# Kernel tuning notes

Measured on AMD Instinct MI355X. Metric: run time of the kernel, lower is better.

Reference implementation:

```python
import jax, jax.numpy as jnp
import numpy as np

B, S, T = 32, 512, 32
EMB, HID = 256, 512
VOCAB, OOV = 50000, 100


def setup_inputs() -> dict:
    key = jax.random.key(0)
    ks = jax.random.split(key, 20)
    g = lambda k, shape: (0.02 * jax.random.normal(k, shape)).astype(jnp.float32)
    return {
        "dec_input_ids": jax.random.randint(ks[0], (B, T), 0, VOCAB),
        "enc_ids_ext": jax.random.randint(ks[1], (B, S), 0, VOCAB + OOV),
        "encoder_states": jax.random.normal(ks[2], (B, S, HID), jnp.float32),
        "enc_padding_mask": jnp.ones((B, S), jnp.float32),
        "init_h": jax.random.normal(ks[3], (B, HID), jnp.float32),
        "init_c": jax.random.normal(ks[4], (B, HID), jnp.float32),
        "embeddings": g(ks[5], (VOCAB, EMB)),
        "W_enc": g(ks[6], (HID, HID)),
        "b_enc": jnp.zeros((HID,), jnp.float32),
        "W_attn": g(ks[7], (2 * HID, HID)),
        "v": g(ks[8], (HID,)),
        "w_cov": g(ks[9], (HID,)),
        "b_cov": jnp.zeros((HID,), jnp.float32),
        "W_x": g(ks[10], (EMB + HID, HID)),
        "W_out": g(ks[11], (2 * HID, HID)),
        "Wk": g(ks[12], (HID, 4 * HID)),
        "Wr": g(ks[13], (HID, 4 * HID)),
        "b_lstm": jnp.zeros((4 * HID,), jnp.float32),
        "W_pgen": g(ks[14], (4 * HID, 1)),
        "W_proj": g(ks[15], (HID, VOCAB)),
        "b_proj": jnp.zeros((VOCAB,), jnp.float32),
    }


def reference(dec_input_ids, enc_ids_ext, encoder_states, enc_padding_mask,
              init_h, init_c, embeddings, W_enc, b_enc, W_attn, v, w_cov,
              b_cov, W_x, W_out, Wk, Wr, b_lstm, W_pgen, W_proj, b_proj):
    Bq = encoder_states.shape[0]
    # 1x1 conv over [B,S,1,H] == pointwise linear
    enc_feat = jnp.einsum('bsh,hv->bsv', encoder_states, W_enc) + b_enc  # [B,S,V]
    emb = jnp.swapaxes(embeddings[dec_input_ids], 0, 1)  # [T,B,E]
    rows = jnp.arange(Bq)[:, None]

    def lstm(x, h, c):
        z = x @ Wk + h @ Wr + b_lstm
        i, f, g_, o = jnp.split(z, 4, axis=-1)
        c2 = jax.nn.sigmoid(f) * c + jax.nn.sigmoid(i) * jnp.tanh(g_)
        h2 = jax.nn.sigmoid(o) * jnp.tanh(c2)
        return h2, c2

    def attend(h, c, cov):
        dec_feat = jnp.concatenate([h, c], -1) @ W_attn  # [B,V]
        feats = enc_feat + dec_feat[:, None, :]
        if cov is not None:  # 1x1 conv on coverage [B,S,1,1] -> [B,S,V]
            feats = feats + cov[..., None] * w_cov + b_cov
        e = jnp.sum(v * jnp.tanh(feats), -1)  # [B,S]
        attn = jax.nn.softmax(e, axis=-1) * enc_padding_mask
        attn = attn / jnp.sum(attn, -1, keepdims=True)
        ctx = jnp.einsum('bs,bsv->bv', attn, enc_feat)
        return ctx, attn

    def decode(inp, h, c, ctx, cov):
        x = jnp.concatenate([inp, ctx], -1) @ W_x
        h, c = lstm(x, h, c)
        ctx, attn = attend(h, c, cov)
        p_gen = jax.nn.sigmoid(jnp.concatenate([ctx, h, c, x], -1) @ W_pgen)  # [B,1]
        out = jnp.concatenate([h, ctx], -1) @ W_out
        vocab_dist = jax.nn.softmax(out @ W_proj + b_proj, axis=-1)
        ext = jnp.concatenate([p_gen * vocab_dist,
                               jnp.zeros((Bq, OOV), vocab_dist.dtype)], -1)
        final = ext.at[rows, enc_ids_ext].add((1.0 - p_gen) * attn)
        return h, c, ctx, attn, p_gen, final

    # step 0: coverage starts as None, initialized from first attn dist
    ctx0 = jnp.zeros((Bq, HID), encoder_states.dtype)
    h, c, ctx, attn0, pg0, final0 = decode(emb[0], init_h, init_c, ctx0, None)
    cov = attn0

    def scan_step(carry, inp):
        h, c, ctx, cov = carry
        h, c, ctx, attn, pg, final = decode(inp, h, c, ctx, cov)
        return (h, c, ctx, cov + attn), final

    (_, _, _, cov), finals = jax.lax.scan(scan_step, (h, c, ctx, cov), emb[1:])
    final_dists = jnp.concatenate([final0[None], finals], axis=0)  # [T,B,VOCAB+OOV]
    return final_dists
```

## Files before the change

kernel.cpp:

```cpp
#include <hip/hip_runtime.h>
#include <math.h>

#define Bq 32
#define Sq 512
#define Tq 32
#define EMBq 256
#define HIDq 512
#define VOCABq 50000
#define OOVq 100
#define VEXTq (VOCABq + OOVq)
#define HALF_N 25088

typedef unsigned short u16;
typedef unsigned long long u64;
typedef __attribute__((ext_vector_type(8))) short bf16x8;
typedef __attribute__((ext_vector_type(4))) float f32x4;

__device__ __forceinline__ float sigmoidf_(float x){ return 1.0f/(1.0f+__expf(-x)); }
__device__ __forceinline__ float tanhf_(float x){ return 1.0f - 2.0f/(__expf(2.0f*x)+1.0f); }

__device__ __forceinline__ u16 f2bf(float x){
  union{float f; unsigned u;} v; v.f=x;
  unsigned r = v.u + 0x7FFFu + ((v.u>>16)&1u);
  return (u16)(r>>16);
}
__device__ __forceinline__ float bf2f(u16 h){
  union{unsigned u; float f;} v; v.u = ((unsigned)h)<<16; return v.f;
}

__device__ __forceinline__ float ld1(const float* p){
  return __hip_atomic_load((float*)p, __ATOMIC_RELAXED, __HIP_MEMORY_SCOPE_AGENT);
}
__device__ __forceinline__ void st1(float* p, float v){
  __hip_atomic_store(p, v, __ATOMIC_RELAXED, __HIP_MEMORY_SCOPE_AGENT);
}
__device__ __forceinline__ float2 ld2(const float* p){
  u64 v = __hip_atomic_load((u64*)p, __ATOMIC_RELAXED, __HIP_MEMORY_SCOPE_AGENT);
  union{u64 u; float2 f;} c; c.u=v; return c.f;
}
__device__ __forceinline__ void atadd(float* p, float v){
  __hip_atomic_fetch_add(p, v, __ATOMIC_RELAXED, __HIP_MEMORY_SCOPE_AGENT);
}

__device__ __forceinline__ void mbar(unsigned* gs, int sc, unsigned tag){
  asm volatile("s_waitcnt vmcnt(0)" ::: "memory");
  __syncthreads();
  if (threadIdx.x==0)
    __hip_atomic_store(gs+sc, tag, __ATOMIC_RELAXED, __HIP_MEMORY_SCOPE_AGENT);
  if (threadIdx.x<64){
    for(;;){
      unsigned v = (threadIdx.x<8)
        ? __hip_atomic_load(gs+threadIdx.x, __ATOMIC_RELAXED, __HIP_MEMORY_SCOPE_AGENT)
        : tag;
      if (__all(v>=tag)) break;
      __builtin_amdgcn_s_sleep(1);
    }
  }
  __syncthreads();
}

__device__ __forceinline__ float blockSum512(float v, float* red){
  #pragma unroll
  for (int off=32; off>0; off>>=1) v += __shfl_down(v, off);
  int lane = threadIdx.x & 63, wid = threadIdx.x >> 6;
  __syncthreads();
  if (lane==0) red[wid]=v;
  __syncthreads();
  float t=0.f;
  #pragma unroll
  for (int w=0;w<8;++w) t+=red[w];
  return t;
}

__global__ __launch_bounds__(256) void k_prep(
    const float* __restrict__ W_enc, u16* __restrict__ WET,
    const float* __restrict__ Wk,    u16* __restrict__ WkT,
    const float* __restrict__ W_out, u16* __restrict__ WoT,
    const float* __restrict__ W_attn,u16* __restrict__ WAbf){
  __shared__ float T[32][33];
  const int bid = blockIdx.x, tid = threadIdx.x;
  if (bid < 1792){
    const float* in; u16* out; int ldin, ldout, n0, k0;
    if (bid < 256){ in=W_enc; out=WET; ldin=512; ldout=512;
      n0=(bid&15)*32; k0=(bid>>4)*32; }
    else if (bid < 1280){ int b=bid-256; in=Wk; out=WkT; ldin=2048; ldout=512;
      n0=(b&63)*32; k0=(b>>6)*32; }
    else { int b=bid-1280; in=W_out; out=WoT; ldin=512; ldout=1024;
      n0=(b&15)*32; k0=(b>>4)*32; }
    #pragma unroll
    for (int it=0; it<4; ++it){
      int id=tid+it*256; int kk=id>>5, nn=id&31;
      T[kk][nn] = in[(size_t)(k0+kk)*ldin + n0+nn];
    }
    __syncthreads();
    #pragma unroll
    for (int it=0; it<4; ++it){
      int id=tid+it*256; int nn=id>>5, kk=id&31;
      out[(size_t)(n0+nn)*ldout + k0+kk] = f2bf(T[kk][nn]);
    }
  } else {
    int i = (bid-1792)*256 + tid;
    WAbf[i] = f2bf(W_attn[i]);
  }
}

__global__ __launch_bounds__(512) void k_wx2c(const float* __restrict__ W_x,
    const float* __restrict__ Wpgen, u16* __restrict__ Xb, float* __restrict__ Wxp){
  __shared__ float red[8];
  const int j = blockIdx.x, i = threadIdx.x;
  float v = W_x[(size_t)(256+j)*512 + i];
  Xb[(size_t)j*512 + i] = f2bf(v);
  float s = blockSum512(v*Wpgen[1536+i], red);
  if (i==0) Wxp[j] = s;
}

__global__ __launch_bounds__(256) void k_gemm512(const u16* __restrict__ A,
    const u16* __restrict__ B, const float* __restrict__ bias,
    float* __restrict__ out, int ncols, int use_bias){
  __shared__ u16 As[128*40];
  __shared__ u16 Bs[128*40];
  const int tid = threadIdx.x;
  const int m0 = blockIdx.x * 128;
  const int n0 = blockIdx.y * 128;
  const int wid = tid>>6, lane = tid&63;
  const int wm = (wid>>1)*64, wn = (wid&1)*64;
  const int l15 = lane&15, l4 = lane>>4;
  f32x4 acc[4][4];
  #pragma unroll
  for (int mi=0;mi<4;++mi)
    #pragma unroll
    for (int ni=0;ni<4;++ni) acc[mi][ni] = (f32x4){0.f,0.f,0.f,0.f};
  for (int kt=0; kt<16; ++kt){
    const int k0 = kt*32;
    __syncthreads();
    #pragma unroll
    for (int it=0; it<2; ++it){
      int id = tid + it*256;
      int row = id>>2, c4 = id&3;
      uint4 va = *(const uint4*)(A + (size_t)(m0+row)*512 + k0 + c4*8);
      *(uint4*)(&As[row*40 + c4*8]) = va;
      uint4 vb = *(const uint4*)(B + (size_t)(n0+row)*512 + k0 + c4*8);
      *(uint4*)(&Bs[row*40 + c4*8]) = vb;
    }
    __syncthreads();
    bf16x8 a[4], b[4];
    #pragma unroll
    for (int mi=0;mi<4;++mi) a[mi] = *(const bf16x8*)(&As[(wm+mi*16+l15)*40 + l4*8]);
    #pragma unroll
    for (int ni=0;ni<4;++ni) b[ni] = *(const bf16x8*)(&Bs[(wn+ni*16+l15)*40 + l4*8]);
    #pragma unroll
    for (int mi=0;mi<4;++mi)
      #pragma unroll
      for (int ni=0;ni<4;++ni)
        acc[mi][ni] = __builtin_amdgcn_mfma_f32_16x16x32_bf16(a[mi], b[ni], acc[mi][ni], 0,0,0);
  }
  #pragma unroll
  for (int ni=0;ni<4;++ni){
    const int col = n0 + wn + ni*16 + l15;
    const float bp = use_bias ? bias[col] : 0.f;
    #pragma unroll
    for (int mi=0;mi<4;++mi){
      const int rbase = m0 + wm + mi*16 + l4*4;
      #pragma unroll
      for (int r=0;r<4;++r)
        out[(size_t)(rbase+r)*ncols + col] = acc[mi][ni][r] + bp;
    }
  }
}

__global__ __launch_bounds__(256) void k_gemmb(const u16* __restrict__ A,
    const u16* __restrict__ B, u16* __restrict__ out, int K, int N){
  __shared__ u16 As[128*40];
  __shared__ u16 Bs[128*40];
  const int tid = threadIdx.x;
  const int m0 = blockIdx.x * 128;
  const int n0 = blockIdx.y * 128;
  const int wid = tid>>6, lane = tid&63;
  const int wm = (wid>>1)*64, wn = (wid&1)*64;
  const int l15 = lane&15, l4 = lane>>4;
  f32x4 acc[4][4];
  #pragma unroll
  for (int mi=0;mi<4;++mi)
    #pragma unroll
    for (int ni=0;ni<4;++ni) acc[mi][ni] = (f32x4){0.f,0.f,0.f,0.f};
  const int kts = K>>5;
  for (int kt=0; kt<kts; ++kt){
    const int k0 = kt*32;
    __syncthreads();
    #pragma unroll
    for (int it=0; it<2; ++it){
      int id = tid + it*256;
      int row = id>>2, c4 = id&3;
      uint4 va = *(const uint4*)(A + (size_t)(m0+row)*K + k0 + c4*8);
      *(uint4*)(&As[row*40 + c4*8]) = va;
      uint4 vb = *(const uint4*)(B + (size_t)(n0+row)*K + k0 + c4*8);
      *(uint4*)(&Bs[row*40 + c4*8]) = vb;
    }
    __syncthreads();
    bf16x8 a[4], b[4];
    #pragma unroll
    for (int mi=0;mi<4;++mi) a[mi] = *(const bf16x8*)(&As[(wm+mi*16+l15)*40 + l4*8]);
    #pragma unroll
    for (int ni=0;ni<4;++ni) b[ni] = *(const bf16x8*)(&Bs[(wn+ni*16+l15)*40 + l4*8]);
    #pragma unroll
    for (int mi=0;mi<4;++mi)
      #pragma unroll
      for (int ni=0;ni<4;++ni)
        acc[mi][ni] = __builtin_amdgcn_mfma_f32_16x16x32_bf16(a[mi], b[ni], acc[mi][ni], 0,0,0);
  }
  #pragma unroll
  for (int ni=0;ni<4;++ni){
    const int col = n0 + wn + ni*16 + l15;
    #pragma unroll
    for (int mi=0;mi<4;++mi){
      const int rbase = m0 + wm + mi*16 + l4*4;
      #pragma unroll
      for (int r=0;r<4;++r)
        out[(size_t)(rbase+r)*N + col] = f2bf(acc[mi][ni][r]);
    }
  }
}

__global__ __launch_bounds__(256) void k_encm(const float* __restrict__ es,
    const u16* __restrict__ WET, const float* __restrict__ b_enc,
    u16* __restrict__ EFbf){
  __shared__ u16 As[128*40];
  __shared__ u16 Bs[128*40];
  const int tid=threadIdx.x;
  const int m0 = blockIdx.x*128, n0 = blockIdx.y*128;
  const int wid=tid>>6, lane=tid&63;
  const int wm=(wid>>1)*64, wn=(wid&1)*64;
  const int l15=lane&15, l4=lane>>4;
  f32x4 acc[4][4];
  #pragma unroll
  for (int mi=0;mi<4;++mi)
    #pragma unroll
    for (int ni=0;ni<4;++ni) acc[mi][ni] = (f32x4){0.f,0.f,0.f,0.f};
  for (int kt=0; kt<16; ++kt){
    const int k0=kt*32;
    __syncthreads();
    #pragma unroll
    for (int it=0; it<4; ++it){
      int id=tid+it*256; int row=id>>3, q=id&7;
      float4 v = *(const float4*)(es + (size_t)(m0+row)*512 + k0 + q*4);
      u64 pk = (u64)f2bf(v.x) | ((u64)f2bf(v.y)<<16) | ((u64)f2bf(v.z)<<32) | ((u64)f2bf(v.w)<<48);
      *(u64*)&As[row*40 + q*4] = pk;
    }
    #pragma unroll
    for (int it=0; it<2; ++it){
      int id=tid+it*256; int row=id>>2, c4=id&3;
      uint4 v = *(const uint4*)(WET + (size_t)(n0+row)*512 + k0 + c4*8);
      *(uint4*)&Bs[row*40 + c4*8] = v;
    }
    __syncthreads();
    bf16x8 a[4], b[4];
    #pragma unroll
    for (int mi=0;mi<4;++mi) a[mi] = *(const bf16x8*)(&As[(wm+mi*16+l15)*40 + l4*8]);
    #pragma unroll
    for (int ni=0;ni<4;++ni) b[ni] = *(const bf16x8*)(&Bs[(wn+ni*16+l15)*40 + l4*8]);
    #pragma unroll
    for (int mi=0;mi<4;++mi)
      #pragma unroll
      for (int ni=0;ni<4;++ni)
        acc[mi][ni] = __builtin_amdgcn_mfma_f32_16x16x32_bf16(a[mi], b[ni], acc[mi][ni], 0,0,0);
  }
  #pragma unroll
  for (int ni=0;ni<4;++ni){
    const int col = n0+wn+ni*16+l15;
    const float bp = b_enc[col];
    #pragma unroll
    for (int mi=0;mi<4;++mi){
      const int rb = m0+wm+mi*16+l4*4;
      #pragma unroll
      for (int r=0;r<4;++r)
        EFbf[(size_t)(rb+r)*512 + col] = f2bf(acc[mi][ni][r]+bp);
    }
  }
}

__global__ __launch_bounds__(512) void k_embx(const int* __restrict__ dec_ids,
  const float* __restrict__ emb, const float* __restrict__ W_x,
  const float* __restrict__ Wpgen, u16* __restrict__ embx_bf, float* __restrict__ embxp){
  __shared__ float A[16][257];
  __shared__ int ids[16];
  __shared__ float red[8];
  const int tid = threadIdx.x, r0 = blockIdx.x*16;
  if (tid<16){
    int row = r0+tid, tt = row>>5, bb = row&31;
    ids[tid] = dec_ids[bb*Tq + tt];
  }
  __syncthreads();
  for (int idx=tid; idx<16*256; idx+=512){
    int rr = idx>>8, kk = idx&255;
    A[rr][kk] = emb[(size_t)ids[rr]*EMBq + kk];
  }
  __syncthreads();
  float acc[16];
  #pragma unroll
  for (int r=0;r<16;++r) acc[r]=0.f;
  for (int k=0;k<256;++k){
    float w = W_x[(size_t)k*HIDq + tid];
    #pragma unroll
    for (int r=0;r<16;++r) acc[r] += A[r][k]*w;
  }
  float wp4 = Wpgen[1536+tid];
  for (int r=0;r<16;++r){
    embx_bf[(size_t)(r0+r)*HIDq + tid] = f2bf(acc[r]);
    float s = blockSum512(acc[r]*wp4, red);
    if (tid==0) embxp[r0+r] = s;
  }
}

__global__ __launch_bounds__(512) void k_trans(const float* __restrict__ in,
    float* __restrict__ out, int K, int N){
  __shared__ float T[32][33];
  const int n0 = blockIdx.x*32, k0 = blockIdx.y*32;
  const int tid = threadIdx.x;
  for (int idx=tid; idx<1024; idx+=512){
    int kk = idx>>5, nn = idx&31;
    T[kk][nn] = in[(size_t)(k0+kk)*N + n0+nn];
  }
  __syncthreads();
  for (int idx=tid; idx<1024; idx+=512){
    int nn = idx>>5, kk = idx&31;
    out[(size_t)(n0+nn)*K + k0+kk] = T[kk][nn];
  }
}

__global__ __launch_bounds__(512) void k_wgc(const float* __restrict__ WXKT_,
    const float* __restrict__ WrT_, u16* __restrict__ WGC){
  const int np = blockIdx.x;
  const int colg = np>>2, g = np&3;
  const int n = g*512 + colg;
  const int sc = np>>8, npl = np&255;
  u16* o = WGC + (size_t)sc*262144 + (size_t)npl*8;
  const int k = threadIdx.x;
  float v0 = WXKT_[(size_t)n*512 + k];
  float v1 = WrT_[(size_t)n*512 + k];
  o[(size_t)(k>>3)*2048 + (k&7)] = f2bf(v0);
  const int k2 = k + 512;
  o[(size_t)(k2>>3)*2048 + (k2&7)] = f2bf(v1);
}

__global__ __launch_bounds__(1024,1) void k_rec9(
  const u16* __restrict__ EFbf, const float* __restrict__ mask,
  const float* __restrict__ init_h, const float* __restrict__ init_c,
  const u16* __restrict__ WGC, const float* __restrict__ embz,
  const u16* __restrict__ WAbf, const float* __restrict__ vvec,
  const float* __restrict__ wcov, const float* __restrict__ bcov,
  const float* __restrict__ Wpgen, const float* __restrict__ Wxp,
  float* __restrict__ Hg, float* __restrict__ ctx_acc,
  float* __restrict__ df_acc, float* __restrict__ Z_acc,
  u16* __restrict__ hc_bf, float* __restrict__ attn_ws,
  float* __restrict__ pgen_raw, unsigned* __restrict__ msl)
{
  __shared__ float xA[1024];
  __shared__ float zl4[4][256];
  __shared__ float hsl[64], csl[64];
  __shared__ float covb[64], wsv[64], coldv[64];
  __shared__ float dfp[1024];
  __shared__ float dfl[512];
  __shared__ float ctp[1024];
  __shared__ float el[64];
  __shared__ float Zsh;

  const int tid = threadIdx.x, bid = blockIdx.x;
  const int lane = tid&63, wv = tid>>6;
  const int sc = bid & 7, bB = bid >> 3, s0 = sc*64;
  const int j0l = lane*8;
  unsigned* gs = msl + bB*16;

  float vvr[8], wcr[8], bcr[8];
  *(float4*)&vvr[0] = *(const float4*)&vvec[j0l]; *(float4*)&vvr[4] = *(const float4*)&vvec[j0l+4];
  *(float4*)&wcr[0] = *(const float4*)&wcov[j0l]; *(float4*)&wcr[4] = *(const float4*)&wcov[j0l+4];
  *(float4*)&bcr[0] = *(const float4*)&bcov[j0l]; *(float4*)&bcr[4] = *(const float4*)&bcov[j0l+4];

  if (tid<64) csl[tid] = init_c[bB*512 + s0 + tid];

  const int colL = tid & 255;
  const int kq = tid >> 8;
  const u16* wbase = WGC + (size_t)sc*262144 + (size_t)(kq*32)*2048 + (size_t)colL*8;
  const float* xs = &xA[kq*256];

  unsigned mt = 0;

  for (int t=0; t<Tq; ++t){
    if (t==0){
      if (tid<512) xA[tid] = 0.f;
      else xA[tid] = init_h[bB*512 + (tid-512)];
      if (tid<64) st1(ctx_acc + bB*512 + s0+tid, 0.f);
      if (tid==0 && sc==0) st1(Z_acc + bB, 0.f);
      __syncthreads();
    } else {
      const int pr = (t-1)&1;
      float2 cf, hf; float Zl = 0.f;
      if (tid<256) cf = ld2(ctx_acc + (size_t)pr*16384 + bB*512 + tid*2);
      else if (tid<512) hf = ld2(Hg + (size_t)pr*16384 + bB*512 + (tid-256)*2);
      if (tid==0)  Zl = ld1(Z_acc + pr*32 + bB);
      if (tid<64)  coldv[tid] = xA[s0+tid];
      if (tid==0)  Zsh = Zl;
      __syncthreads();
      const float Z = Zsh;
      if (tid<256){ xA[tid*2] = cf.x/Z; xA[tid*2+1] = cf.y/Z; }
      else if (tid<512){ xA[512+(tid-256)*2] = hf.x; xA[512+(tid-256)*2+1] = hf.y; }
      __syncthreads();
      if (tid<64){
        const int j = s0+tid;
        float cxj = xA[j];
        __builtin_nontemporal_store(f2bf(cxj), hc_bf + ((size_t)(t-1)*Bq+bB)*1024 + 512 + j);
        float a = wsv[tid]/Z;
        __builtin_nontemporal_store(a, attn_ws + ((size_t)(t-1)*Bq+bB)*Sq + j);
        covb[tid] = (t==1) ? a : covb[tid]+a;
        float part = cxj*Wpgen[j] + hsl[tid]*Wpgen[512+j]
                   + csl[tid]*Wpgen[1024+j] + coldv[tid]*Wxp[j];
        #pragma unroll
        for (int off=32; off>0; off>>=1) part += __shfl_down(part, off);
        if (tid==0) atadd(pgen_raw + (t-1)*Bq + bB, part);
      }
      if (tid<64) st1(ctx_acc + (size_t)(t&1)*16384 + bB*512 + s0+tid, 0.f);
      if (tid==0 && sc==0) st1(Z_acc + (t&1)*32 + bB, 0.f);
      __syncthreads();
    }
    {
      float acc = 0.f;
      #pragma unroll 8
      for (int kb=0; kb<32; ++kb){
        bf16x8 w8 = *(const bf16x8*)(wbase + (size_t)kb*2048);
        const u16* ph = (const u16*)&w8;
        float4 x0 = *(const float4*)(xs + kb*8);
        float4 x1 = *(const float4*)(xs + kb*8 + 4);
        acc += x0.x*bf2f(ph[0]) + x0.y*bf2f(ph[1]) + x0.z*bf2f(ph[2]) + x0.w*bf2f(ph[3])
             + x1.x*bf2f(ph[4]) + x1.y*bf2f(ph[5]) + x1.z*bf2f(ph[6]) + x1.w*bf2f(ph[7]);
      }
      zl4[kq][colL] = acc;
    }
    __syncthreads();
    if (tid<64){
      const int colg = s0 + tid;
      const float* ez = embz + ((size_t)t*Bq + bB)*2048 + colg;
      float zi = (zl4[0][tid*4+0]+zl4[1][tid*4+0])+(zl4[2][tid*4+0]+zl4[3][tid*4+0])
               + __builtin_nontemporal_load(ez);
      float zf = (zl4[0][tid*4+1]+zl4[1][tid*4+1])+(zl4[2][tid*4+1]+zl4[3][tid*4+1])
               + __builtin_nontemporal_load(ez+512);
      float zg = (zl4[0][tid*4+2]+zl4[1][tid*4+2])+(zl4[2][tid*4+2]+zl4[3][tid*4+2])
               + __builtin_nontemporal_load(ez+1024);
      float zo = (zl4[0][tid*4+3]+zl4[1][tid*4+3])+(zl4[2][tid*4+3]+zl4[3][tid*4+3])
               + __builtin_nontemporal_load(ez+1536);
      float co = csl[tid];
      float cn = sigmoidf_(zf)*co + sigmoidf_(zi)*tanhf_(zg);
      float hn = sigmoidf_(zo)*tanhf_(cn);
      csl[tid] = cn;
      hsl[tid] = hn;
      st1(Hg + (size_t)(t&1)*16384 + bB*512 + colg, hn);
      __builtin_nontemporal_store(f2bf(hn), hc_bf + ((size_t)t*Bq+bB)*1024 + colg);
    }
    __syncthreads();
    {
      const int j = tid & 511, half = tid >> 9;
      const float* st = half ? csl : hsl;
      const u16* wa = WAbf + (size_t)(half*512 + s0)*512 + j;
      float acc = 0.f;
      #pragma unroll 8
      for (int k=0;k<64;++k) acc += st[k]*bf2f(wa[(size_t)k*512]);
      dfp[tid] = acc;
    }
    __syncthreads();
    if (tid<512) atadd(df_acc + (size_t)(t&1)*16384 + bB*512 + tid, dfp[tid]+dfp[512+tid]);
    ++mt; mbar(gs, sc, mt);
    if (tid<256){
      float2 f = ld2(df_acc + (size_t)(t&1)*16384 + bB*512 + tid*2);
      dfl[tid*2]=f.x; dfl[tid*2+1]=f.y;
    } else if (tid>=960){
      st1(df_acc + (size_t)((t+1)&1)*16384 + bB*512 + s0 + (tid-960), 0.f);
    }
    __syncthreads();
    {
      float dd[8];
      *(float4*)&dd[0] = *(const float4*)&dfl[j0l];
      *(float4*)&dd[4] = *(const float4*)&dfl[j0l+4];
      const u16* efb = EFbf + ((size_t)(bB*512 + s0))*512;
      #pragma unroll
      for (int r=0;r<4;++r){
        int sl = wv*4 + r;
        uint4 pack = *(const uint4*)(efb + (size_t)sl*512 + j0l);
        const u16* ph = (const u16*)&pack;
        float a8 = 0.f;
        if (t>0){
          float cvs = covb[sl];
          #pragma unroll
          for (int q=0;q<8;++q) a8 += vvr[q]*tanhf_(bf2f(ph[q])+dd[q]+cvs*wcr[q]+bcr[q]);
        } else {
          #pragma unroll
          for (int q=0;q<8;++q) a8 += vvr[q]*tanhf_(bf2f(ph[q])+dd[q]);
        }
        #pragma unroll
        for (int off=32; off>0; off>>=1) a8 += __shfl_down(a8, off);
        if (lane==0) el[sl] = a8;
      }
    }
    __syncthreads();
    if (tid<64){
      float w_ = mask[bB*512+s0+tid]*__expf(el[tid]);
      wsv[tid] = w_;
      float Zc = w_;
      #pragma unroll
      for (int off=32; off>0; off>>=1) Zc += __shfl_xor(Zc, off);
      if (tid==0) atadd(Z_acc + (t&1)*32 + bB, Zc);
    }
    __syncthreads();
    {
      const int j = tid & 511, sh = tid >> 9;
      const u16* efc = EFbf + ((size_t)(bB*512 + s0 + sh*32))*512 + j;
      float acc = 0.f;
      #pragma unroll 4
      for (int s=0;s<32;++s) acc += wsv[sh*32+s]*bf2f(efc[(size_t)s*512]);
      ctp[tid] = acc;
    }
    __syncthreads();
    if (tid<512) atadd(ctx_acc + (size_t)(t&1)*16384 + bB*512 + tid, ctp[tid]+ctp[512+tid]);
    ++mt; mbar(gs, sc, mt);
  }
  {
    const int pr = (Tq-1)&1;
    float2 cf; float Zl = 0.f;
    if (tid<256) cf = ld2(ctx_acc + (size_t)pr*16384 + bB*512 + tid*2);
    if (tid==0)  Zl = ld1(Z_acc + pr*32 + bB);
    if (tid<64)  coldv[tid] = xA[s0+tid];
    if (tid==0)  Zsh = Zl;
    __syncthreads();
    const float Z = Zsh;
    if (tid<256){ xA[tid*2] = cf.x/Z; xA[tid*2+1] = cf.y/Z; }
    __syncthreads();
    if (tid<64){
      const int j = s0+tid;
      float cxj = xA[j];
      __builtin_nontemporal_store(f2bf(cxj), hc_bf + ((size_t)(Tq-1)*Bq+bB)*1024 + 512 + j);
      float a = wsv[tid]/Z;
      __builtin_nontemporal_store(a, attn_ws + ((size_t)(Tq-1)*Bq+bB)*Sq + j);
      float part = cxj*Wpgen[j] + hsl[tid]*Wpgen[512+j]
                 + csl[tid]*Wpgen[1024+j] + coldv[tid]*Wxp[j];
      #pragma unroll
      for (int off=32; off>0; off>>=1) part += __shfl_down(part, off);
      if (tid==0) atadd(pgen_raw + (Tq-1)*Bq + bB, part);
    }
  }
}

__global__ __launch_bounds__(256) void k_wcvt(const float* __restrict__ Wp,
    u16* __restrict__ WT, int n_base){
  __shared__ float T[32][33];
  const int n0 = blockIdx.x*32, k0 = blockIdx.y*32;
  const int tid = threadIdx.x;
  #pragma unroll
  for (int it=0; it<4; ++it){
    int id = tid + it*256;
    int kk = id>>5, nn = id&31;
    int gn = n_base + n0 + nn;
    T[kk][nn] = (gn < VOCABq) ? Wp[(size_t)(k0+kk)*VOCABq + gn] : 0.f;
  }
  __syncthreads();
  #pragma unroll
  for (int it=0; it<4; ++it){
    int id = tid + it*256;
    int nn = id>>5, kk = id&31;
    WT[(size_t)(n0+nn)*512 + k0+kk] = f2bf(T[kk][nn]);
  }
}

__global__ __launch_bounds__(256) void k_projs(const u16* __restrict__ Abf,
    const u16* __restrict__ WT, const float* __restrict__ b_proj,
    float* __restrict__ out, float* __restrict__ rowsum, int n_base){
  __shared__ u16 As[128*40];
  __shared__ u16 Bs[128*40];
  const int tid = threadIdx.x;
  const int m0 = blockIdx.x * 128;
  const int n0 = blockIdx.y * 128;
  const int wid = tid>>6, lane = tid&63;
  const int wm = (wid>>1)*64, wn = (wid&1)*64;
  const int l15 = lane&15, l4 = lane>>4;
  f32x4 acc[4][4];
  #pragma unroll
  for (int mi=0;mi<4;++mi)
    #pragma unroll
    for (int ni=0;ni<4;++ni) acc[mi][ni] = (f32x4){0.f,0.f,0.f,0.f};

  for (int kt=0; kt<16; ++kt){
    const int k0 = kt*32;
    __syncthreads();
    #pragma unroll
    for (int it=0; it<2; ++it){
      int id = tid + it*256;
      int row = id>>2, c4 = id&3;
      uint4 va = *(const uint4*)(Abf + (size_t)(m0+row)*512 + k0 + c4*8);
      *(uint4*)(&As[row*40 + c4*8]) = va;
      uint4 vb = *(const uint4*)(WT + (size_t)(n0+row)*512 + k0 + c4*8);
      *(uint4*)(&Bs[row*40 + c4*8]) = vb;
    }
    __syncthreads();
    bf16x8 a[4], b[4];
    #pragma unroll
    for (int mi=0;mi<4;++mi)
      a[mi] = *(const bf16x8*)(&As[(wm + mi*16 + l15)*40 + l4*8]);
    #pragma unroll
    for (int ni=0;ni<4;++ni)
      b[ni] = *(const bf16x8*)(&Bs[(wn + ni*16 + l15)*40 + l4*8]);
    #pragma unroll
    for (int mi=0;mi<4;++mi)
      #pragma unroll
      for (int ni=0;ni<4;++ni)
        acc[mi][ni] = __builtin_amdgcn_mfma_f32_16x16x32_bf16(a[mi], b[ni], acc[mi][ni], 0,0,0);
  }

  float prow[4][4];
  #pragma unroll
  for (int mi=0;mi<4;++mi)
    #pragma unroll
    for (int r=0;r<4;++r) prow[mi][r]=0.f;

  #pragma unroll
  for (int ni=0;ni<4;++ni){
    const int col = n_base + n0 + wn + ni*16 + l15;
    const bool ok = (col < VOCABq);
    const float bp = ok ? b_proj[col] : 0.f;
    #pragma unroll
    for (int mi=0;mi<4;++mi){
      const int rbase = m0 + wm + mi*16 + l4*4;
      #pragma unroll
      for (int r=0;r<4;++r){
        float p = ok ? __expf(acc[mi][ni][r] + bp) : 0.f;
        if (ok) out[(size_t)(rbase+r)*VEXTq + col] = p;
        prow[mi][r] += p;
      }
    }
  }
  #pragma unroll
  for (int mi=0;mi<4;++mi)
    #pragma unroll
    for (int r=0;r<4;++r){
      float v = prow[mi][r];
      v += __shfl_xor(v,1); v += __shfl_xor(v,2);
      v += __shfl_xor(v,4); v += __shfl_xor(v,8);
      if (l15==0) atadd(rowsum + m0 + wm + mi*16 + l4*4 + r, v);
    }
}

__global__ __launch_bounds__(256) void k_sm2(float* __restrict__ out,
    const float* __restrict__ rowsum, const float* __restrict__ pgen_raw,
    const float* __restrict__ embxp, const float* __restrict__ attn_ws,
    const int* __restrict__ enc_ids){
  const int row=blockIdx.x, tid=threadIdx.x;
  const int b = row & (Bq-1);
  float* orow = out + (size_t)row*VEXTq;
  const float pg = sigmoidf_(pgen_raw[row] + embxp[row]);
  const float scale = pg / rowsum[row];
  float4* o4 = (float4*)orow;
  for (int i=tid;i<VOCABq/4;i+=256){
    float4 v = o4[i];
    v.x*=scale; v.y*=scale; v.z*=scale; v.w*=scale;
    o4[i] = v;
  }
  for (int i=VOCABq+tid;i<VEXTq;i+=256) orow[i] = 0.f;
  __syncthreads();
  const float w1 = 1.f-pg;
  const float* arow = attn_ws + (size_t)row*Sq;
  const int* ids = enc_ids + b*Sq;
  for (int si=tid; si<Sq; si+=256)
    atomicAdd(&orow[ids[si]], w1*arow[si]);
}

extern "C" void kernel_launch(void* const* d_in, const int* in_sizes, int n_in,
                              void* d_out, int out_size, void* d_ws, size_t ws_size,
                              hipStream_t stream) {
  (void)in_sizes; (void)n_in; (void)out_size; (void)ws_size;
  const int*   dec_ids    = (const int*)  d_in[0];
  const int*   enc_ids    = (const int*)  d_in[1];
  const float* enc_states = (const float*)d_in[2];
  const float* mask       = (const float*)d_in[3];
  const float* init_h     = (const float*)d_in[4];
  const float* init_c     = (const float*)d_in[5];
  const float* embeddings = (const float*)d_in[6];
  const float* W_enc      = (const float*)d_in[7];
  const float* b_enc      = (const float*)d_in[8];
  const float* W_attn     = (const float*)d_in[9];
  const float* vvec       = (const float*)d_in[10];
  const float* w_cov      = (const float*)d_in[11];
  const float* b_cov      = (const float*)d_in[12];
  const float* W_x        = (const float*)d_in[13];
  const float* W_out      = (const float*)d_in[14];
  const float* Wk         = (const float*)d_in[15];
  const float* Wr         = (const float*)d_in[16];
  const float* b_lstm     = (const float*)d_in[17];
  const float* W_pgen     = (const float*)d_in[18];
  const float* W_proj     = (const float*)d_in[19];
  const float* b_proj     = (const float*)d_in[20];
  float* out = (float*)d_out;
  float* ws  = (float*)d_ws;

  u16*   EFbf    = (u16*)ws;
  float* attn_ws = ws + 4194304;
  u16*   hc_bf   = (u16*)(attn_ws + 524288);
  u16*   outm_bf = (u16*)(attn_ws + 524288 + 524288);
  u16*   embx_bf = (u16*)(attn_ws + 524288 + 524288 + 262144);
  float* embxp   = attn_ws + 524288 + 524288 + 262144 + 262144;
  float* embz    = embxp + 1024;
  float* WXKT_   = embz + 2097152;
  float* WrT_    = WXKT_ + 1048576;
  u16*   WkT     = (u16*)(WrT_ + 1048576);
  u16*   Xb      = (u16*)(((float*)WkT) + 524288);
  u16*   WoT     = (u16*)(((float*)Xb) + 131072);
  float* Wxp     = ((float*)WoT) + 262144;
  float* Hg      = Wxp + 512;
  unsigned* msl  = (unsigned*)(Hg + 32768);
  float* pgen_raw= (float*)(msl + 512);
  float* ctx_acc = pgen_raw + 1024;
  float* df_acc  = ctx_acc + 32768;
  float* Z_acc   = df_acc + 32768;
  float* rowsum  = Z_acc + 64;
  u16*   WGC     = (u16*)(rowsum + 1024);
  u16*   WAbf    = (u16*)(((float*)WGC) + 1048576);
  u16*   WET     = (u16*)(((float*)WAbf) + 262144);
  u16*   WT      = (u16*)(((float*)WET) + 131072);

  hipMemsetAsync(msl, 0, (512 + 1024 + 32768 + 32768 + 64 + 1024)*sizeof(unsigned), stream);

  k_prep<<<3840, 256, 0, stream>>>(W_enc, WET, Wk, WkT, W_out, WoT, W_attn, WAbf);
  {
    dim3 g(128,4);
    k_encm<<<g, 256, 0, stream>>>(enc_states, WET, b_enc, EFbf);
  }
  k_embx<<<64, 512, 0, stream>>>(dec_ids, embeddings, W_x, W_pgen, embx_bf, embxp);
  k_wx2c<<<512, 512, 0, stream>>>(W_x, W_pgen, Xb, Wxp);
  {
    dim3 g(8,16);
    k_gemm512<<<g, 256, 0, stream>>>(embx_bf, WkT, b_lstm, embz, 2048, 1);
  }
  {
    dim3 g(16,4);
    k_gemm512<<<g, 256, 0, stream>>>(WkT, Xb, (const float*)0, WXKT_, 512, 0);
  }
  {
    dim3 g(64,16);
    k_trans<<<g, 512, 0, stream>>>(Wr, WrT_, 512, 2048);
  }
  k_wgc<<<2048, 512, 0, stream>>>(WXKT_, WrT_, WGC);

  {
    void* args[] = { (void*)&EFbf, (void*)&mask, (void*)&init_h, (void*)&init_c,
                     (void*)&WGC, (void*)&embz, (void*)&WAbf, (void*)&vvec,
                     (void*)&w_cov, (void*)&b_cov, (void*)&W_pgen, (void*)&Wxp,
                     (void*)&Hg, (void*)&ctx_acc, (void*)&df_acc, (void*)&Z_acc,
                     (void*)&hc_bf, (void*)&attn_ws, (void*)&pgen_raw,
                     (void*)&msl };
    hipLaunchCooperativeKernel((void*)k_rec9, dim3(256), dim3(1024), args, 0, stream);
  }

  {
    dim3 g(8,4);
    k_gemmb<<<g, 256, 0, stream>>>(hc_bf, WoT, outm_bf, 1024, 512);
  }
  for (int half=0; half<2; ++half){
    const int n_base = half*HALF_N;
    dim3 gc(HALF_N/32, 16);
    k_wcvt<<<gc, 256, 0, stream>>>(W_proj, WT, n_base);
    dim3 gp(8, HALF_N/128);
    k_projs<<<gp, 256, 0, stream>>>(outm_bf, WT, b_proj, out, rowsum, n_base);
  }
  k_sm2<<<Tq*Bq, 256, 0, stream>>>(out, rowsum, pgen_raw, embxp, attn_ws, enc_ids);
}
```

Measured before the change: 1.425 ms.

## Fuse W_proj fp32-to-bf16 conversion into the vocab projection GEMM

Removes the separate transpose/convert kernel that wrote a bf16 transposed copy of W_proj, and has the projection GEMM load fp32 W_proj directly, converting to bf16 and transposing into shared memory. The two half launches become one grid covering the full vocabulary. This saves a write and re-read of the 51 MB weight copy. In exchange, each of the 8 M-blocks now rereads the fp32 weights (twice the bytes of bf16), and the scattered 2-byte shared stores may cause bank conflicts.

```diff
diff --git a/kernel.cpp b/kernel.cpp
--- a/kernel.cpp
+++ b/kernel.cpp
@@ -9,7 +9,6 @@
 #define VOCABq 50000
 #define OOVq 100
 #define VEXTq (VOCABq + OOVq)
-#define HALF_N 25088
 
 typedef unsigned short u16;
 typedef unsigned long long u64;
@@ -332,14 +331,14 @@
   const int np = blockIdx.x;
   const int colg = np>>2, g = np&3;
   const int n = g*512 + colg;
+  const float* s1 = WXKT_ + (size_t)n*512;
+  const float* s2 = WrT_  + (size_t)n*512;
   const int sc = np>>8, npl = np&255;
   u16* o = WGC + (size_t)sc*262144 + (size_t)npl*8;
   const int k = threadIdx.x;
-  float v0 = WXKT_[(size_t)n*512 + k];
-  float v1 = WrT_[(size_t)n*512 + k];
-  o[(size_t)(k>>3)*2048 + (k&7)] = f2bf(v0);
+  o[(size_t)(k>>3)*2048 + (k&7)] = f2bf(s1[k]);
   const int k2 = k + 512;
-  o[(size_t)(k2>>3)*2048 + (k2&7)] = f2bf(v1);
+  o[(size_t)(k2>>3)*2048 + (k2&7)] = f2bf(s2[k]);
 }
 
 __global__ __launch_bounds__(1024,1) void k_rec9(
@@ -546,30 +545,9 @@
   }
 }
 
-__global__ __launch_bounds__(256) void k_wcvt(const float* __restrict__ Wp,
-    u16* __restrict__ WT, int n_base){
-  __shared__ float T[32][33];
-  const int n0 = blockIdx.x*32, k0 = blockIdx.y*32;
-  const int tid = threadIdx.x;
-  #pragma unroll
-  for (int it=0; it<4; ++it){
-    int id = tid + it*256;
-    int kk = id>>5, nn = id&31;
-    int gn = n_base + n0 + nn;
-    T[kk][nn] = (gn < VOCABq) ? Wp[(size_t)(k0+kk)*VOCABq + gn] : 0.f;
-  }
-  __syncthreads();
-  #pragma unroll
-  for (int it=0; it<4; ++it){
-    int id = tid + it*256;
-    int nn = id>>5, kk = id&31;
-    WT[(size_t)(n0+nn)*512 + k0+kk] = f2bf(T[kk][nn]);
-  }
-}
-
-__global__ __launch_bounds__(256) void k_projs(const u16* __restrict__ Abf,
-    const u16* __restrict__ WT, const float* __restrict__ b_proj,
-    float* __restrict__ out, float* __restrict__ rowsum, int n_base){
+__global__ __launch_bounds__(256) void k_projsf(const u16* __restrict__ Abf,
+    const float* __restrict__ Wp, const float* __restrict__ b_proj,
+    float* __restrict__ out, float* __restrict__ rowsum){
   __shared__ u16 As[128*40];
   __shared__ u16 Bs[128*40];
   const int tid = threadIdx.x;
@@ -593,8 +571,26 @@
       int row = id>>2, c4 = id&3;
       uint4 va = *(const uint4*)(Abf + (size_t)(m0+row)*512 + k0 + c4*8);
       *(uint4*)(&As[row*40 + c4*8]) = va;
-      uint4 vb = *(const uint4*)(WT + (size_t)(n0+row)*512 + k0 + c4*8);
-      *(uint4*)(&Bs[row*40 + c4*8]) = vb;
+    }
+    #pragma unroll
+    for (int it=0; it<4; ++it){
+      int id = tid + it*256;
+      int kk = id>>5;
+      int nn4 = (id&31)*4;
+      int gn = n0 + nn4;
+      const float* src = Wp + (size_t)(k0+kk)*VOCABq + gn;
+      float4 v;
+      if (gn+3 < VOCABq) v = *(const float4*)src;
+      else {
+        v.x = (gn+0<VOCABq)? src[0] : 0.f;
+        v.y = (gn+1<VOCABq)? src[1] : 0.f;
+        v.z = (gn+2<VOCABq)? src[2] : 0.f;
+        v.w = (gn+3<VOCABq)? src[3] : 0.f;
+      }
+      Bs[(nn4+0)*40 + kk] = f2bf(v.x);
+      Bs[(nn4+1)*40 + kk] = f2bf(v.y);
+      Bs[(nn4+2)*40 + kk] = f2bf(v.z);
+      Bs[(nn4+3)*40 + kk] = f2bf(v.w);
     }
     __syncthreads();
     bf16x8 a[4], b[4];
@@ -619,7 +615,7 @@
 
   #pragma unroll
   for (int ni=0;ni<4;++ni){
-    const int col = n_base + n0 + wn + ni*16 + l15;
+    const int col = n0 + wn + ni*16 + l15;
     const bool ok = (col < VOCABq);
     const float bp = ok ? b_proj[col] : 0.f;
     #pragma unroll
@@ -719,7 +715,6 @@
   u16*   WGC     = (u16*)(rowsum + 1024);
   u16*   WAbf    = (u16*)(((float*)WGC) + 1048576);
   u16*   WET     = (u16*)(((float*)WAbf) + 262144);
-  u16*   WT      = (u16*)(((float*)WET) + 131072);
 
   hipMemsetAsync(msl, 0, (512 + 1024 + 32768 + 32768 + 64 + 1024)*sizeof(unsigned), stream);
 
@@ -758,12 +753,9 @@
     dim3 g(8,4);
     k_gemmb<<<g, 256, 0, stream>>>(hc_bf, WoT, outm_bf, 1024, 512);
   }
-  for (int half=0; half<2; ++half){
-    const int n_base = half*HALF_N;
-    dim3 gc(HALF_N/32, 16);
-    k_wcvt<<<gc, 256, 0, stream>>>(W_proj, WT, n_base);
-    dim3 gp(8, HALF_N/128);
-    k_projs<<<gp, 256, 0, stream>>>(outm_bf, WT, b_proj, out, rowsum, n_base);
+  {
+    dim3 gp(8, 391);
+    k_projsf<<<gp, 256, 0, stream>>>(outm_bf, W_proj, b_proj, out, rowsum);
   }
   k_sm2<<<Tq*Bq, 256, 0, stream>>>(out, rowsum, pgen_raw, embxp, attn_ws, enc_ids);
 }
```

Measured after the change: 1.495 ms. +5.0%, slower.
